# Optimization experiments

Measured on AMD Instinct MI355X. Metric: run time of the kernel, lower is better.

Reference implementation:

```python
import jax, jax.numpy as jnp
import numpy as np

B, T, C, H, MEM = 2, 2048, 1024, 16, 256
HD = C // H


def setup_inputs() -> dict:
    key = jax.random.key(0)
    ks = jax.random.split(key, 6)
    return {
        "x": jax.random.normal(ks[0], (B, T, C), dtype=jnp.float32),
        "ext_mem": jax.random.normal(ks[1], (B, MEM, C), dtype=jnp.float32),
        "W_attn": jax.random.normal(ks[2], (C, 3 * C), dtype=jnp.float32) * 0.02,
        "b_attn": jax.random.normal(ks[3], (3 * C,), dtype=jnp.float32) * 0.02,
        "W_proj": jax.random.normal(ks[4], (C, C), dtype=jnp.float32) * 0.02,
        "b_proj": jax.random.normal(ks[5], (C,), dtype=jnp.float32) * 0.02,
    }


def reference(x, ext_mem, W_attn, b_attn, W_proj, b_proj):
    Bx, Tx, Cx = x.shape
    qkv = x @ W_attn + b_attn                      # [B,T,3C]
    q, k, v = jnp.split(qkv, 3, axis=-1)
    # [B,H,T,HD]
    q = q.reshape(Bx, Tx, H, HD).transpose(0, 2, 1, 3)
    k = k.reshape(Bx, Tx, H, HD).transpose(0, 2, 1, 3)
    v = v.reshape(Bx, Tx, H, HD).transpose(0, 2, 1, 3)
    mem = ext_mem.reshape(Bx, -1, H, HD).transpose(0, 2, 1, 3)  # [B,H,MEM,HD]
    k = jnp.concatenate([mem, k], axis=2)          # [B,H,MEM+T,HD]
    v = jnp.concatenate([mem, v], axis=2)
    mem_len = k.shape[2] - Tx
    scale = 1.0 / jnp.sqrt(jnp.float32(HD))
    att = jnp.einsum("bhtd,bhsd->bhts", q, k) * scale  # [B,H,T,MEM+T]
    # memory prefix fully attended; causal over the T query positions
    rows = jnp.arange(Tx)[:, None]
    cols = jnp.arange(mem_len + Tx)[None, :]
    allowed = (cols < mem_len) | ((cols - mem_len) <= rows)  # [T,MEM+T]
    att = jnp.where(allowed[None, None], att, jnp.float32(-jnp.inf))
    att = jax.nn.softmax(att, axis=-1)
    y = jnp.einsum("bhts,bhsd->bhtd", att, v)      # [B,H,T,HD]
    y = y.transpose(0, 2, 1, 3).reshape(Bx, Tx, Cx)
    return y @ W_proj + b_proj
```

## Files before the change

kernel.cpp:

```cpp
#include <hip/hip_runtime.h>

#define B_    2
#define T_    2048
#define C_    1024
#define H_    16
#define HD_   64
#define MEM_  256
#define S_    2304
#define NKT_  36

typedef __attribute__((ext_vector_type(8))) short short8;
typedef __attribute__((ext_vector_type(4))) float f32x4;

__device__ __forceinline__ unsigned short f2bf(float x) {
    return (unsigned short)((__float_as_uint(x) + 0x8000u) >> 16);
}

typedef const __attribute__((address_space(1))) unsigned int* gp_t;
typedef __attribute__((address_space(3))) unsigned int* lp_t;

__device__ __forceinline__ void gll16(const unsigned short* g, unsigned short* l) {
    __builtin_amdgcn_global_load_lds((gp_t)g, (lp_t)l, 16, 0, 0);
}

__global__ __launch_bounds__(256) void convert_x_tiled(
    const float* __restrict__ in, unsigned short* __restrict__ out)
{
    int i = blockIdx.x * 256 + threadIdx.x;
    int c = (i & 255) * 4;
    int m = i >> 8;
    float4 v = ((const float4*)in)[i];
    ushort4 o;
    o.x = f2bf(v.x); o.y = f2bf(v.y); o.z = f2bf(v.z); o.w = f2bf(v.w);
    int mt = m >> 7, r = m & 127, kc = c >> 5, cc = c & 31;
    int p = (cc >> 3) ^ ((r >> 1) & 3);
    *(ushort4*)&out[(((size_t)mt * 32 + kc) << 12) + (r << 5) + p * 8 + (cc & 7)] = o;
}

__global__ __launch_bounds__(256) void transpose_w_tiled(
    const float* __restrict__ in, unsigned short* __restrict__ out, int Cc)
{
    __shared__ float L[64][65];
    const int tid = threadIdx.x;
    const int r0 = blockIdx.y * 64, c0 = blockIdx.x * 64;
    const int jj = tid >> 4;
    const int i4 = (tid & 15) * 4;
#pragma unroll
    for (int t = 0; t < 4; ++t) {
        int j = jj + t * 16;
        float4 v = *(const float4*)(in + (size_t)(r0 + j) * Cc + c0 + i4);
        L[i4 + 0][j] = v.x; L[i4 + 1][j] = v.y;
        L[i4 + 2][j] = v.z; L[i4 + 3][j] = v.w;
    }
    __syncthreads();
#pragma unroll
    for (int t = 0; t < 4; ++t) {
        int n = c0 + jj + t * 16;
        int k = r0 + i4;
        ushort4 o;
        o.x = f2bf(L[jj + t * 16][i4 + 0]); o.y = f2bf(L[jj + t * 16][i4 + 1]);
        o.z = f2bf(L[jj + t * 16][i4 + 2]); o.w = f2bf(L[jj + t * 16][i4 + 3]);
        int nt = n >> 7, r = n & 127, kc = k >> 5, cc = k & 31;
        int p = (cc >> 3) ^ ((r >> 1) & 3);
        *(ushort4*)&out[(((size_t)nt * 32 + kc) << 12) + (r << 5) + p * 8 + (cc & 7)] = o;
    }
}

__global__ __launch_bounds__(256) void mem_copy_bf(
    const float* __restrict__ ext,
    unsigned short* __restrict__ k_ws, unsigned short* __restrict__ v_tl)
{
    int idx = blockIdx.x * 256 + threadIdx.x;
    float val = ext[idx];
    int c = idx & (C_ - 1), m = (idx >> 10) & (MEM_ - 1), b = idx >> 18;
    int h = c >> 6, d = c & 63;
    int bh = b * H_ + h;
    unsigned short bv = f2bf(val);
    k_ws[(size_t)bh * S_ * 64 + (size_t)m * 64 + (((d >> 3) ^ (m & 7)) << 3) + (d & 7)] = bv;
    int ts = m >> 6, key = m & 63;
    v_tl[(((size_t)bh * NKT_ + ts) * 64 + d) * 64 + (((key >> 3) ^ (d & 7)) << 3) + (key & 7)] = bv;
}

template<int MODE>
__global__ __launch_bounds__(256) void gemm_mfma(
    const unsigned short* __restrict__ A,
    const unsigned short* __restrict__ Bt,
    const float* __restrict__ bias,
    unsigned short* __restrict__ q_ws,
    unsigned short* __restrict__ k_ws,
    unsigned short* __restrict__ v_tl,
    float* __restrict__ out)
{
    __shared__ __align__(16) unsigned short As[2][4096];
    __shared__ __align__(16) unsigned short Bs[2][4096];
    const int tid = threadIdx.x, lane = tid & 63, wave = tid >> 6;
    const int wr = wave >> 1, wc = wave & 1;
    const size_t abase = (size_t)blockIdx.y * 32 * 4096;
    const size_t bbase = (size_t)blockIdx.x * 32 * 4096;

    f32x4 acc[4][4];
#pragma unroll
    for (int i = 0; i < 4; ++i)
#pragma unroll
        for (int j = 0; j < 4; ++j) acc[i][j] = (f32x4){0.f, 0.f, 0.f, 0.f};

    auto stage = [&](int kc, int buf) {
        const unsigned short* ga = A + abase + (size_t)kc * 4096;
        const unsigned short* gb = Bt + bbase + (size_t)kc * 4096;
#pragma unroll
        for (int s = 0; s < 2; ++s) {
            int seg = wave + s * 4;
            gll16(ga + seg * 512 + lane * 8, &As[buf][seg * 512]);
            gll16(gb + seg * 512 + lane * 8, &Bs[buf][seg * 512]);
        }
    };

    stage(0, 0);
    __syncthreads();
    for (int kc = 0; kc < 32; ++kc) {
        if (kc + 1 < 32) stage(kc + 1, (kc + 1) & 1);
        const unsigned short* as = As[kc & 1];
        const unsigned short* bs = Bs[kc & 1];
        short8 af[4], bf4[4];
#pragma unroll
        for (int i = 0; i < 4; ++i) {
            int row = wr * 64 + i * 16 + (lane & 15);
            int ph = (lane >> 4) ^ ((row >> 1) & 3);
            af[i] = *(const short8*)&as[row * 32 + ph * 8];
        }
#pragma unroll
        for (int j = 0; j < 4; ++j) {
            int row = wc * 64 + j * 16 + (lane & 15);
            int ph = (lane >> 4) ^ ((row >> 1) & 3);
            bf4[j] = *(const short8*)&bs[row * 32 + ph * 8];
        }
#pragma unroll
        for (int i = 0; i < 4; ++i)
#pragma unroll
            for (int j = 0; j < 4; ++j)
                acc[i][j] = __builtin_amdgcn_mfma_f32_16x16x32_bf16(
                    af[i], bf4[j], acc[i][j], 0, 0, 0);
        __syncthreads();
    }

    if (MODE == 0) {
#pragma unroll
        for (int j = 0; j < 4; ++j) {
            int n = blockIdx.x * 128 + wc * 64 + j * 16 + (lane & 15);
            float bs = bias[n];
            int sel = n >> 10, h = (n >> 6) & 15, d = n & 63;
#pragma unroll
            for (int i = 0; i < 4; ++i) {
                int m = blockIdx.y * 128 + wr * 64 + i * 16 + (lane >> 4) * 4;
                int b = m >> 11, t0 = m & (T_ - 1);
                int bh = b * H_ + h;
                if (sel == 0) {
                    size_t base = ((size_t)bh * T_ + t0) * 64 + d;
#pragma unroll
                    for (int r = 0; r < 4; ++r)
                        q_ws[base + (size_t)r * 64] = f2bf(acc[i][j][r] + bs);
                } else if (sel == 1) {
#pragma unroll
                    for (int r = 0; r < 4; ++r) {
                        int s = MEM_ + t0 + r;
                        k_ws[(size_t)bh * S_ * 64 + (size_t)s * 64
                             + (((d >> 3) ^ (s & 7)) << 3) + (d & 7)] =
                            f2bf(acc[i][j][r] + bs);
                    }
                } else {
                    int s0 = MEM_ + t0, ts = s0 >> 6, key = s0 & 63;
                    ushort4 pv;
                    pv.x = f2bf(acc[i][j][0] + bs);
                    pv.y = f2bf(acc[i][j][1] + bs);
                    pv.z = f2bf(acc[i][j][2] + bs);
                    pv.w = f2bf(acc[i][j][3] + bs);
                    *(ushort4*)&v_tl[(((size_t)bh * NKT_ + ts) * 64 + d) * 64
                                     + (((key >> 3) ^ (d & 7)) << 3) + (key & 7)] = pv;
                }
            }
        }
    } else {
#pragma unroll
        for (int j = 0; j < 4; ++j) {
            int n = blockIdx.x * 128 + wc * 64 + j * 16 + (lane & 15);
            float bs = bias[n];
#pragma unroll
            for (int i = 0; i < 4; ++i) {
                int m = blockIdx.y * 128 + wr * 64 + i * 16 + (lane >> 4) * 4;
#pragma unroll
                for (int r = 0; r < 4; ++r)
                    out[(size_t)(m + r) * C_ + n] = acc[i][j][r] + bs;
            }
        }
    }
}

__global__ __launch_bounds__(256) void flash_mfma(
    const unsigned short* __restrict__ qg,
    const unsigned short* __restrict__ kg,
    const unsigned short* __restrict__ vg,
    unsigned short* __restrict__ yt)
{
    __shared__ __align__(16) unsigned short Ks[2][4096];
    __shared__ __align__(16) unsigned short Vs[2][4096];
    __shared__ unsigned short Ps[4][16][72];

    const int tid = threadIdx.x, lane = tid & 63, wave = tid >> 6;
    const int a = blockIdx.x;
    const int h = blockIdx.y, b = blockIdx.z;
    const int qtA = a, qtB = 31 - a;
    const int ntA = 5 + qtA, ntB = 5 + qtB;
    const int bh = b * H_ + h;
    const size_t kbase = (size_t)bh * S_ * 64;
    const size_t vbase = (size_t)bh * NKT_ * 4096;

    short8 qfA[2], qfB[2];
    {
        const unsigned short* p = qg + ((size_t)bh * T_ + qtA * 64 + wave * 16
                                        + (lane & 15)) * 64 + (lane >> 4) * 8;
        qfA[0] = *(const short8*)p; qfA[1] = *(const short8*)(p + 32);
        p = qg + ((size_t)bh * T_ + qtB * 64 + wave * 16
                  + (lane & 15)) * 64 + (lane >> 4) * 8;
        qfB[0] = *(const short8*)p; qfB[1] = *(const short8*)(p + 32);
    }

    f32x4 oA[4], oB[4];
#pragma unroll
    for (int j = 0; j < 4; ++j) {
        oA[j] = (f32x4){0.f, 0.f, 0.f, 0.f};
        oB[j] = (f32x4){0.f, 0.f, 0.f, 0.f};
    }
    float lA[4] = {0.f, 0.f, 0.f, 0.f}, lB[4] = {0.f, 0.f, 0.f, 0.f};

    auto stage = [&](int kt, int buf) {
        const unsigned short* gk = kg + kbase + (size_t)kt * 4096;
        const unsigned short* gv = vg + vbase + (size_t)kt * 4096;
#pragma unroll
        for (int s = 0; s < 2; ++s) {
            int seg = wave + s * 4;
            gll16(gk + seg * 512 + lane * 8, &Ks[buf][seg * 512]);
            gll16(gv + seg * 512 + lane * 8, &Vs[buf][seg * 512]);
        }
    };

    const float C1 = 0.18033688011112042f;

    auto process = [&](const short8* qf, f32x4* o, float* l, int qt0, bool diag,
                       const unsigned short* ks, const unsigned short* vs, int s0) {
        f32x4 sc[4];
#pragma unroll
        for (int kb = 0; kb < 4; ++kb) {
            int key = kb * 16 + (lane & 15);
            short8 k0 = *(const short8*)&ks[key * 64 + (((lane >> 4)    ) ^ (key & 7)) * 8];
            short8 k1 = *(const short8*)&ks[key * 64 + (((lane >> 4) + 4) ^ (key & 7)) * 8];
            f32x4 z = (f32x4){0.f, 0.f, 0.f, 0.f};
            z = __builtin_amdgcn_mfma_f32_16x16x32_bf16(qf[0], k0, z, 0, 0, 0);
            z = __builtin_amdgcn_mfma_f32_16x16x32_bf16(qf[1], k1, z, 0, 0, 0);
            sc[kb] = z;
        }
#pragma unroll
        for (int kb = 0; kb < 4; ++kb)
#pragma unroll
            for (int r = 0; r < 4; ++r) {
                float pv = exp2f(sc[kb][r] * C1);
                if (diag) {
                    int sg = s0 + kb * 16 + (lane & 15);
                    int t = qt0 + wave * 16 + (lane >> 4) * 4 + r;
                    if (sg - MEM_ > t) pv = 0.f;
                }
                l[r] += pv;
                Ps[wave][(lane >> 4) * 4 + r][kb * 16 + (lane & 15)] = f2bf(pv);
            }
        short8 pa0 = *(const short8*)&Ps[wave][lane & 15][(lane >> 4) * 8];
        short8 pa1 = *(const short8*)&Ps[wave][lane & 15][32 + (lane >> 4) * 8];
#pragma unroll
        for (int j = 0; j < 4; ++j) {
            int d = j * 16 + (lane & 15);
            short8 v0 = *(const short8*)&vs[d * 64 + (((lane >> 4)    ) ^ (d & 7)) * 8];
            short8 v1 = *(const short8*)&vs[d * 64 + (((lane >> 4) + 4) ^ (d & 7)) * 8];
            o[j] = __builtin_amdgcn_mfma_f32_16x16x32_bf16(pa0, v0, o[j], 0, 0, 0);
            o[j] = __builtin_amdgcn_mfma_f32_16x16x32_bf16(pa1, v1, o[j], 0, 0, 0);
        }
    };

    stage(0, 0);
    __syncthreads();
    for (int kt = 0; kt < ntB; ++kt) {
        const int buf = kt & 1;
        if (kt + 1 < ntB) stage(kt + 1, buf ^ 1);
        const unsigned short* ks = Ks[buf];
        const unsigned short* vs = Vs[buf];
        const int s0 = kt * 64;
        if (kt < ntA) process(qfA, oA, lA, qtA * 64, kt == ntA - 1, ks, vs, s0);
        process(qfB, oB, lB, qtB * 64, kt == ntB - 1, ks, vs, s0);
        __syncthreads();
    }

    auto finish = [&](f32x4* o, float* l, int qt0) {
#pragma unroll
        for (int j = 0; j < 4; ++j) {
            int d = j * 16 + (lane & 15);
#pragma unroll
            for (int r = 0; r < 4; ++r) {
                float s = l[r];
                if (j == 0) {
                    s += __shfl_xor(s, 1); s += __shfl_xor(s, 2);
                    s += __shfl_xor(s, 4); s += __shfl_xor(s, 8);
                    l[r] = s;
                }
                int t = qt0 + wave * 16 + (lane >> 4) * 4 + r;
                float y = o[j][r] / l[r];
                int m = b * T_ + t, c = h * 64 + d;
                int mt = m >> 7, rr = m & 127, kc = c >> 5, cc = c & 31;
                int p = (cc >> 3) ^ ((rr >> 1) & 3);
                yt[(((size_t)mt * 32 + kc) << 12) + (rr << 5) + p * 8 + (cc & 7)] = f2bf(y);
            }
        }
    };
    finish(oA, lA, qtA * 64);
    finish(oB, lB, qtB * 64);
}

extern "C" void kernel_launch(void* const* d_in, const int* in_sizes, int n_in,
                              void* d_out, int out_size, void* d_ws, size_t ws_size,
                              hipStream_t stream) {
    (void)in_sizes; (void)n_in; (void)out_size; (void)ws_size;
    const float* x      = (const float*)d_in[0];
    const float* ext    = (const float*)d_in[1];
    const float* W_attn = (const float*)d_in[2];
    const float* b_attn = (const float*)d_in[3];
    const float* W_proj = (const float*)d_in[4];
    const float* b_proj = (const float*)d_in[5];
    float* out = (float*)d_out;

    unsigned short* x_tl  = (unsigned short*)d_ws;
    unsigned short* WtA   = x_tl + 4194304;
    unsigned short* WtP   = WtA + 3145728;
    unsigned short* q_ws  = WtP + 1048576;
    unsigned short* k_ws  = q_ws + 4194304;
    unsigned short* v_tl  = k_ws + 4718592;
    unsigned short* y_tl  = v_tl + 4718592;

    dim3 blk(256);
    convert_x_tiled<<<4096, blk, 0, stream>>>(x, x_tl);
    transpose_w_tiled<<<dim3(48, 16), blk, 0, stream>>>(W_attn, WtA, 3 * C_);
    transpose_w_tiled<<<dim3(16, 16), blk, 0, stream>>>(W_proj, WtP, C_);
    gemm_mfma<0><<<dim3(24, 32), blk, 0, stream>>>(
        x_tl, WtA, b_attn, q_ws, k_ws, v_tl, nullptr);
    mem_copy_bf<<<2048, blk, 0, stream>>>(ext, k_ws, v_tl);
    flash_mfma<<<dim3(16, H_, B_), blk, 0, stream>>>(q_ws, k_ws, v_tl, y_tl);
    gemm_mfma<1><<<dim3(8, 32), blk, 0, stream>>>(
        y_tl, WtP, b_proj, nullptr, nullptr, nullptr, out);
}
```

Before: 222.3 us.

## Keep attention probabilities in registers via transposed MFMA and merge prep kernels

The flash kernel computes S^T (K as the A operand), so each lane's exp outputs form a 16x16x16 MFMA A-fragment directly. This removes the per-wave LDS round trip for P. K and V fragments are loaded once per tile and shared by both query tiles, and the row sum shrinks to one scalar per lane. The x conversion, both weight transposes and the memory-prefix copy are merged into one launch to cut launch overhead. The cost is higher register pressure from holding the kA and vB fragments.

```diff
diff --git a/kernel.cpp b/kernel.cpp
--- a/kernel.cpp
+++ b/kernel.cpp
@@ -10,12 +10,19 @@
 #define NKT_  36
 
 typedef __attribute__((ext_vector_type(8))) short short8;
+typedef __attribute__((ext_vector_type(4))) short short4v;
 typedef __attribute__((ext_vector_type(4))) float f32x4;
 
 __device__ __forceinline__ unsigned short f2bf(float x) {
     return (unsigned short)((__float_as_uint(x) + 0x8000u) >> 16);
 }
 
+__device__ __forceinline__ unsigned int pk2bf(float lo, float hi) {
+    unsigned int a = __float_as_uint(lo) + 0x8000u;
+    unsigned int b = __float_as_uint(hi) + 0x8000u;
+    return __builtin_amdgcn_perm(b, a, 0x07060302);
+}
+
 typedef const __attribute__((address_space(1))) unsigned int* gp_t;
 typedef __attribute__((address_space(3))) unsigned int* lp_t;
 
@@ -23,62 +30,66 @@
     __builtin_amdgcn_global_load_lds((gp_t)g, (lp_t)l, 16, 0, 0);
 }
 
-__global__ __launch_bounds__(256) void convert_x_tiled(
-    const float* __restrict__ in, unsigned short* __restrict__ out)
-{
-    int i = blockIdx.x * 256 + threadIdx.x;
-    int c = (i & 255) * 4;
-    int m = i >> 8;
-    float4 v = ((const float4*)in)[i];
-    ushort4 o;
-    o.x = f2bf(v.x); o.y = f2bf(v.y); o.z = f2bf(v.z); o.w = f2bf(v.w);
-    int mt = m >> 7, r = m & 127, kc = c >> 5, cc = c & 31;
-    int p = (cc >> 3) ^ ((r >> 1) & 3);
-    *(ushort4*)&out[(((size_t)mt * 32 + kc) << 12) + (r << 5) + p * 8 + (cc & 7)] = o;
-}
-
-__global__ __launch_bounds__(256) void transpose_w_tiled(
-    const float* __restrict__ in, unsigned short* __restrict__ out, int Cc)
+__global__ __launch_bounds__(256) void prep_all(
+    const float* __restrict__ x, const float* __restrict__ Wa,
+    const float* __restrict__ Wp, const float* __restrict__ ext,
+    unsigned short* __restrict__ x_tl, unsigned short* __restrict__ WtA,
+    unsigned short* __restrict__ WtP, unsigned short* __restrict__ k_ws,
+    unsigned short* __restrict__ v_tl)
 {
     __shared__ float L[64][65];
-    const int tid = threadIdx.x;
-    const int r0 = blockIdx.y * 64, c0 = blockIdx.x * 64;
-    const int jj = tid >> 4;
-    const int i4 = (tid & 15) * 4;
-#pragma unroll
-    for (int t = 0; t < 4; ++t) {
-        int j = jj + t * 16;
-        float4 v = *(const float4*)(in + (size_t)(r0 + j) * Cc + c0 + i4);
-        L[i4 + 0][j] = v.x; L[i4 + 1][j] = v.y;
-        L[i4 + 2][j] = v.z; L[i4 + 3][j] = v.w;
-    }
-    __syncthreads();
-#pragma unroll
-    for (int t = 0; t < 4; ++t) {
-        int n = c0 + jj + t * 16;
-        int k = r0 + i4;
+    const int bid = blockIdx.x, tid = threadIdx.x;
+    if (bid < 4096) {
+        int i = bid * 256 + tid;
+        int c = (i & 255) * 4;
+        int m = i >> 8;
+        float4 v = ((const float4*)x)[i];
         ushort4 o;
-        o.x = f2bf(L[jj + t * 16][i4 + 0]); o.y = f2bf(L[jj + t * 16][i4 + 1]);
-        o.z = f2bf(L[jj + t * 16][i4 + 2]); o.w = f2bf(L[jj + t * 16][i4 + 3]);
-        int nt = n >> 7, r = n & 127, kc = k >> 5, cc = k & 31;
+        o.x = f2bf(v.x); o.y = f2bf(v.y); o.z = f2bf(v.z); o.w = f2bf(v.w);
+        int mt = m >> 7, r = m & 127, kc = c >> 5, cc = c & 31;
         int p = (cc >> 3) ^ ((r >> 1) & 3);
-        *(ushort4*)&out[(((size_t)nt * 32 + kc) << 12) + (r << 5) + p * 8 + (cc & 7)] = o;
-    }
-}
-
-__global__ __launch_bounds__(256) void mem_copy_bf(
-    const float* __restrict__ ext,
-    unsigned short* __restrict__ k_ws, unsigned short* __restrict__ v_tl)
-{
-    int idx = blockIdx.x * 256 + threadIdx.x;
-    float val = ext[idx];
-    int c = idx & (C_ - 1), m = (idx >> 10) & (MEM_ - 1), b = idx >> 18;
-    int h = c >> 6, d = c & 63;
-    int bh = b * H_ + h;
-    unsigned short bv = f2bf(val);
-    k_ws[(size_t)bh * S_ * 64 + (size_t)m * 64 + (((d >> 3) ^ (m & 7)) << 3) + (d & 7)] = bv;
-    int ts = m >> 6, key = m & 63;
-    v_tl[(((size_t)bh * NKT_ + ts) * 64 + d) * 64 + (((key >> 3) ^ (d & 7)) << 3) + (key & 7)] = bv;
+        *(ushort4*)&x_tl[(((size_t)mt * 32 + kc) << 12) + (r << 5) + p * 8 + (cc & 7)] = o;
+    } else if (bid < 5120) {
+        const float* in; unsigned short* out; int Cc, r0, c0;
+        if (bid < 4864) {
+            int r = bid - 4096; in = Wa; out = WtA; Cc = 3 * C_;
+            c0 = (r % 48) * 64; r0 = (r / 48) * 64;
+        } else {
+            int r = bid - 4864; in = Wp; out = WtP; Cc = C_;
+            c0 = (r & 15) * 64; r0 = (r >> 4) * 64;
+        }
+        const int jj = tid >> 4;
+        const int i4 = (tid & 15) * 4;
+#pragma unroll
+        for (int t = 0; t < 4; ++t) {
+            int j = jj + t * 16;
+            float4 v = *(const float4*)(in + (size_t)(r0 + j) * Cc + c0 + i4);
+            L[i4 + 0][j] = v.x; L[i4 + 1][j] = v.y;
+            L[i4 + 2][j] = v.z; L[i4 + 3][j] = v.w;
+        }
+        __syncthreads();
+#pragma unroll
+        for (int t = 0; t < 4; ++t) {
+            int n = c0 + jj + t * 16;
+            int k = r0 + i4;
+            ushort4 o;
+            o.x = f2bf(L[jj + t * 16][i4 + 0]); o.y = f2bf(L[jj + t * 16][i4 + 1]);
+            o.z = f2bf(L[jj + t * 16][i4 + 2]); o.w = f2bf(L[jj + t * 16][i4 + 3]);
+            int nt = n >> 7, r = n & 127, kc = k >> 5, cc = k & 31;
+            int p = (cc >> 3) ^ ((r >> 1) & 3);
+            *(ushort4*)&out[(((size_t)nt * 32 + kc) << 12) + (r << 5) + p * 8 + (cc & 7)] = o;
+        }
+    } else {
+        int idx = (bid - 5120) * 256 + tid;
+        float val = ext[idx];
+        int c = idx & (C_ - 1), m = (idx >> 10) & (MEM_ - 1), b = idx >> 18;
+        int h = c >> 6, d = c & 63;
+        int bh = b * H_ + h;
+        unsigned short bv = f2bf(val);
+        k_ws[(size_t)bh * S_ * 64 + (size_t)m * 64 + (((d >> 3) ^ (m & 7)) << 3) + (d & 7)] = bv;
+        int ts = m >> 6, key = m & 63;
+        v_tl[(((size_t)bh * NKT_ + ts) * 64 + d) * 64 + (((key >> 3) ^ (d & 7)) << 3) + (key & 7)] = bv;
+    }
 }
 
 template<int MODE>
@@ -203,9 +214,9 @@
 {
     __shared__ __align__(16) unsigned short Ks[2][4096];
     __shared__ __align__(16) unsigned short Vs[2][4096];
-    __shared__ unsigned short Ps[4][16][72];
 
     const int tid = threadIdx.x, lane = tid & 63, wave = tid >> 6;
+    const int quad = lane >> 4;
     const int a = blockIdx.x;
     const int h = blockIdx.y, b = blockIdx.z;
     const int qtA = a, qtB = 31 - a;
@@ -217,10 +228,10 @@
     short8 qfA[2], qfB[2];
     {
         const unsigned short* p = qg + ((size_t)bh * T_ + qtA * 64 + wave * 16
-                                        + (lane & 15)) * 64 + (lane >> 4) * 8;
+                                        + (lane & 15)) * 64 + quad * 8;
         qfA[0] = *(const short8*)p; qfA[1] = *(const short8*)(p + 32);
         p = qg + ((size_t)bh * T_ + qtB * 64 + wave * 16
-                  + (lane & 15)) * 64 + (lane >> 4) * 8;
+                  + (lane & 15)) * 64 + quad * 8;
         qfB[0] = *(const short8*)p; qfB[1] = *(const short8*)(p + 32);
     }
 
@@ -230,7 +241,7 @@
         oA[j] = (f32x4){0.f, 0.f, 0.f, 0.f};
         oB[j] = (f32x4){0.f, 0.f, 0.f, 0.f};
     }
-    float lA[4] = {0.f, 0.f, 0.f, 0.f}, lB[4] = {0.f, 0.f, 0.f, 0.f};
+    float lA = 0.f, lB = 0.f;
 
     auto stage = [&](int kt, int buf) {
         const unsigned short* gk = kg + kbase + (size_t)kt * 4096;
@@ -244,44 +255,6 @@
     };
 
     const float C1 = 0.18033688011112042f;
-
-    auto process = [&](const short8* qf, f32x4* o, float* l, int qt0, bool diag,
-                       const unsigned short* ks, const unsigned short* vs, int s0) {
-        f32x4 sc[4];
-#pragma unroll
-        for (int kb = 0; kb < 4; ++kb) {
-            int key = kb * 16 + (lane & 15);
-            short8 k0 = *(const short8*)&ks[key * 64 + (((lane >> 4)    ) ^ (key & 7)) * 8];
-            short8 k1 = *(const short8*)&ks[key * 64 + (((lane >> 4) + 4) ^ (key & 7)) * 8];
-            f32x4 z = (f32x4){0.f, 0.f, 0.f, 0.f};
-            z = __builtin_amdgcn_mfma_f32_16x16x32_bf16(qf[0], k0, z, 0, 0, 0);
-            z = __builtin_amdgcn_mfma_f32_16x16x32_bf16(qf[1], k1, z, 0, 0, 0);
-            sc[kb] = z;
-        }
-#pragma unroll
-        for (int kb = 0; kb < 4; ++kb)
-#pragma unroll
-            for (int r = 0; r < 4; ++r) {
-                float pv = exp2f(sc[kb][r] * C1);
-                if (diag) {
-                    int sg = s0 + kb * 16 + (lane & 15);
-                    int t = qt0 + wave * 16 + (lane >> 4) * 4 + r;
-                    if (sg - MEM_ > t) pv = 0.f;
-                }
-                l[r] += pv;
-                Ps[wave][(lane >> 4) * 4 + r][kb * 16 + (lane & 15)] = f2bf(pv);
-            }
-        short8 pa0 = *(const short8*)&Ps[wave][lane & 15][(lane >> 4) * 8];
-        short8 pa1 = *(const short8*)&Ps[wave][lane & 15][32 + (lane >> 4) * 8];
-#pragma unroll
-        for (int j = 0; j < 4; ++j) {
-            int d = j * 16 + (lane & 15);
-            short8 v0 = *(const short8*)&vs[d * 64 + (((lane >> 4)    ) ^ (d & 7)) * 8];
-            short8 v1 = *(const short8*)&vs[d * 64 + (((lane >> 4) + 4) ^ (d & 7)) * 8];
-            o[j] = __builtin_amdgcn_mfma_f32_16x16x32_bf16(pa0, v0, o[j], 0, 0, 0);
-            o[j] = __builtin_amdgcn_mfma_f32_16x16x32_bf16(pa1, v1, o[j], 0, 0, 0);
-        }
-    };
 
     stage(0, 0);
     __syncthreads();
@@ -291,29 +264,80 @@
         const unsigned short* ks = Ks[buf];
         const unsigned short* vs = Vs[buf];
         const int s0 = kt * 64;
-        if (kt < ntA) process(qfA, oA, lA, qtA * 64, kt == ntA - 1, ks, vs, s0);
-        process(qfB, oB, lB, qtB * 64, kt == ntB - 1, ks, vs, s0);
+
+        short8 kA[4][2];
+#pragma unroll
+        for (int kb = 0; kb < 4; ++kb)
+#pragma unroll
+            for (int ksub = 0; ksub < 2; ++ksub) {
+                int key = kb * 16 + (lane & 15);
+                int ph = (ksub * 4 + quad) ^ (lane & 7);
+                kA[kb][ksub] = *(const short8*)&ks[key * 64 + ph * 8];
+            }
+        short4v vB[4][4];
+#pragma unroll
+        for (int kb = 0; kb < 4; ++kb)
+#pragma unroll
+            for (int dblk = 0; dblk < 4; ++dblk) {
+                int d = dblk * 16 + (lane & 15);
+                int ph = (kb * 2 + (lane >> 5)) ^ (d & 7);
+                vB[kb][dblk] = *(const short4v*)&vs[d * 64 + ph * 8 + (quad & 1) * 4];
+            }
+
+        auto process = [&](const short8* qf, f32x4* o, float& l, int qt0, bool diag) {
+#pragma unroll
+            for (int kb = 0; kb < 4; ++kb) {
+                f32x4 z = (f32x4){0.f, 0.f, 0.f, 0.f};
+                z = __builtin_amdgcn_mfma_f32_16x16x32_bf16(kA[kb][0], qf[0], z, 0, 0, 0);
+                z = __builtin_amdgcn_mfma_f32_16x16x32_bf16(kA[kb][1], qf[1], z, 0, 0, 0);
+                float p[4];
+#pragma unroll
+                for (int r = 0; r < 4; ++r) {
+                    float e = exp2f(z[r] * C1);
+                    if (diag) {
+                        int key = s0 + kb * 16 + quad * 4 + r;
+                        int t = qt0 + wave * 16 + (lane & 15);
+                        if (key - MEM_ > t) e = 0.f;
+                    }
+                    l += e;
+                    p[r] = e;
+                }
+                unsigned int r01 = pk2bf(p[0], p[1]);
+                unsigned int r23 = pk2bf(p[2], p[3]);
+                short4v pf;
+                *(unsigned int*)&pf = r01;
+                *((unsigned int*)&pf + 1) = r23;
+#pragma unroll
+                for (int dblk = 0; dblk < 4; ++dblk)
+                    o[dblk] = __builtin_amdgcn_mfma_f32_16x16x16bf16_1k(
+                        pf, vB[kb][dblk], o[dblk], 0, 0, 0);
+            }
+        };
+
+        if (kt < ntA) process(qfA, oA, lA, qtA * 64, kt == ntA - 1);
+        process(qfB, oB, lB, qtB * 64, kt == ntB - 1);
         __syncthreads();
     }
 
-    auto finish = [&](f32x4* o, float* l, int qt0) {
-#pragma unroll
-        for (int j = 0; j < 4; ++j) {
-            int d = j * 16 + (lane & 15);
+    auto finish = [&](f32x4* o, float l, int qt0) {
+        l += __shfl_xor(l, 16);
+        l += __shfl_xor(l, 32);
+        float linv[4];
+#pragma unroll
+        for (int r = 0; r < 4; ++r)
+            linv[r] = 1.f / __shfl(l, quad * 4 + r);
+#pragma unroll
+        for (int dblk = 0; dblk < 4; ++dblk) {
+            int c = h * 64 + dblk * 16 + (lane & 15);
+            int kc = c >> 5, cc = c & 31;
 #pragma unroll
             for (int r = 0; r < 4; ++r) {
-                float s = l[r];
-                if (j == 0) {
-                    s += __shfl_xor(s, 1); s += __shfl_xor(s, 2);
-                    s += __shfl_xor(s, 4); s += __shfl_xor(s, 8);
-                    l[r] = s;
-                }
-                int t = qt0 + wave * 16 + (lane >> 4) * 4 + r;
-                float y = o[j][r] / l[r];
-                int m = b * T_ + t, c = h * 64 + d;
-                int mt = m >> 7, rr = m & 127, kc = c >> 5, cc = c & 31;
+                int t = qt0 + wave * 16 + quad * 4 + r;
+                int m = b * T_ + t;
+                int mt = m >> 7, rr = m & 127;
                 int p = (cc >> 3) ^ ((rr >> 1) & 3);
-                yt[(((size_t)mt * 32 + kc) << 12) + (rr << 5) + p * 8 + (cc & 7)] = f2bf(y);
+                yt[(((size_t)mt * 32 + kc) << 12) + (rr << 5) + p * 8 + (cc & 7)] =
+                    f2bf(o[dblk][r] * linv[r]);
             }
         }
     };
@@ -342,12 +366,10 @@
     unsigned short* y_tl  = v_tl + 4718592;
 
     dim3 blk(256);
-    convert_x_tiled<<<4096, blk, 0, stream>>>(x, x_tl);
-    transpose_w_tiled<<<dim3(48, 16), blk, 0, stream>>>(W_attn, WtA, 3 * C_);
-    transpose_w_tiled<<<dim3(16, 16), blk, 0, stream>>>(W_proj, WtP, C_);
+    prep_all<<<7168, blk, 0, stream>>>(x, W_attn, W_proj, ext,
+                                       x_tl, WtA, WtP, k_ws, v_tl);
     gemm_mfma<0><<<dim3(24, 32), blk, 0, stream>>>(
         x_tl, WtA, b_attn, q_ws, k_ws, v_tl, nullptr);
-    mem_copy_bf<<<2048, blk, 0, stream>>>(ext, k_ws, v_tl);
     flash_mfma<<<dim3(16, H_, B_), blk, 0, stream>>>(q_ws, k_ws, v_tl, y_tl);
     gemm_mfma<1><<<dim3(8, 32), blk, 0, stream>>>(
         y_tl, WtP, b_proj, nullptr, nullptr, nullptr, out);
```

New measurement: 213.5 us. 3.9% less time.
